# Performance work log

Hardware: AMD Instinct MI355X
Metric: run time of the kernel (lower is better)

## Reference

```python
import jax, jax.numpy as jnp
import numpy as np

B = 64      # graphs per batch
N = 1024    # nodes per graph (equal-size graphs -> static top-k)
D = 256     # in_dim
DEG = 16    # avg degree
K = 512     # k = ratio * N, ratio = 0.5
E = B * N * DEG
NT = B * N


def setup_inputs() -> dict:
    key = jax.random.key(0)
    ks = jax.random.split(key, 8)
    feature = jax.random.normal(ks[0], (NT, D), jnp.float32)
    gid = jnp.repeat(jnp.arange(B), N * DEG)          # graph id per edge
    src = gid * N + jax.random.randint(ks[1], (E,), 0, N)
    dst = gid * N + jax.random.randint(ks[2], (E,), 0, N)
    label = jax.random.randint(ks[3], (B,), 0, 2)
    W = jax.random.normal(ks[4], (D, 1), jnp.float32) / np.sqrt(D)   # GraphConv weight
    b = jnp.zeros((1,), jnp.float32)                                  # GraphConv bias
    lin1_w = jax.random.normal(ks[5], (2, 1), jnp.float32) / np.sqrt(2.0)
    lin1_b = jnp.zeros((1,), jnp.float32)
    return dict(feature=feature, src=src, dst=dst, label=label,
                W=W, b=b, lin1_w=lin1_w, lin1_b=lin1_b)


def reference(feature, src, dst, label, W, b, lin1_w, lin1_b):
    fdt = feature.dtype
    # ---- get_bias_score: distance-to-class-center score ----
    node_label = jnp.repeat(label, N).astype(fdt)                 # [NT]
    gemb = feature.reshape(B, N, D).mean(axis=1)                  # AvgPooling per graph [B, D]
    lab_f = label.astype(fdt)                                     # [B]
    n1 = jnp.maximum(lab_f.sum(), 1.0)
    n0 = jnp.maximum((1.0 - lab_f).sum(), 1.0)
    center0 = (gemb * (1.0 - lab_f)[:, None]).sum(0) / n0         # [D]
    center1 = (gemb * lab_f[:, None]).sum(0) / n1                 # [D]
    d0 = jnp.sqrt(((feature - center0) ** 2).sum(-1))             # [NT]
    d1 = jnp.sqrt(((feature - center1) ** 2).sum(-1))             # [NT]
    score_distance = (d0 - d1) * ((node_label - 0.5) * 2.0)       # [NT]
    # ---- GraphConv(in_dim, 1), norm='both' (DGL semantics) ----
    ones_e = jnp.ones((E,), fdt)
    deg_out = jax.ops.segment_sum(ones_e, src, NT)
    deg_in = jax.ops.segment_sum(ones_e, dst, NT)
    ns = jnp.maximum(deg_out, 1.0) ** -0.5                        # src-side norm
    nd = jnp.maximum(deg_in, 1.0) ** -0.5                         # dst-side norm
    h = (feature @ W) * ns[:, None]                               # project first (out<in) [NT,1]
    agg = jax.ops.segment_sum(h[src], dst, NT)                    # [NT,1]
    score_gcn = (agg * nd[:, None] + b)[:, 0]                     # [NT]
    # ---- combine two scores with lin1: Linear(2, 1) ----
    score = jnp.stack([score_gcn, score_distance], axis=-1) @ lin1_w + lin1_b  # [NT,1]
    sflat = score[:, 0]
    # ---- per-graph top-k (mytopk with equal-size graphs -> static k) ----
    _, idx = jax.lax.top_k(sflat.reshape(B, N), K)                # [B,K] local indices
    perm = (idx + (jnp.arange(B) * N)[:, None]).reshape(-1)       # [B*K] global indices
    mask = jnp.ones((NT,), bool).at[perm].set(False)
    perm_com = jnp.nonzero(mask, size=NT - B * K)[0]              # complement, static size
    # ---- gather + tanh-gated features ----
    feature_dis = feature[perm] * jnp.tanh(sflat[perm])[:, None]          # [B*K, D]
    feature_com = feature[perm_com] * jnp.tanh(sflat[perm_com])[:, None]  # [B*(N-K), D]
    score_soft = jax.nn.softmax(score, axis=0)                    # softmax over all nodes
    return feature_dis, feature_com, perm, perm_com, score_soft
```

## Files before the change

### kernel.cpp

```cpp
#include <hip/hip_runtime.h>
#include <math.h>

#define Bg   64
#define Nn   1024
#define Dd   256
#define EPG  16384
#define NT   (Bg * Nn)
#define Kk   512

#define OFF_DIS   0
#define OFF_COM   8388608
#define OFF_PERM  16777216
#define OFF_PCOM  16809984
#define OFF_SOFT  16842752

#define WS_H0     0
#define WS_SFLAT  (NT * 4)
#define WS_GPART  (NT * 4 * 2)
#define WS_REDM   (WS_GPART + 512 * 256 * 4)
#define WS_REDS   (WS_REDM + 256)
#define WS_PERMI  (WS_REDS + 256)
#define WS_PCOMI  (WS_PERMI + 32768 * 4)

__global__ __launch_bounds__(256) void k_col(
        const float* __restrict__ f, const float* __restrict__ W,
        float* __restrict__ gpart, float* __restrict__ h0) {
    __shared__ float scol[1024];
    int blk = blockIdx.x, t = threadIdx.x;
    int base = blk * 128;
    int lane = t & 63, wid = t >> 6;
    const float4* f4 = (const float4*)f;
    const float4* W4 = (const float4*)W;
    float4 w = W4[lane];
    float4 cs = make_float4(0.f, 0.f, 0.f, 0.f);
    for (int r = 0; r < 32; ++r) {
        int row = base + wid * 32 + r;
        float4 v = f4[(size_t)row * 64 + lane];
        cs.x += v.x; cs.y += v.y; cs.z += v.z; cs.w += v.w;
        float d = v.x * w.x + v.y * w.y + v.z * w.z + v.w * w.w;
        for (int o = 32; o > 0; o >>= 1) d += __shfl_xor(d, o);
        if (lane == 0) h0[row] = d;
    }
    ((float4*)scol)[wid * 64 + lane] = cs;
    __syncthreads();
    gpart[blk * Dd + t] = scol[t] + scol[Dd + t] + scol[2 * Dd + t] + scol[3 * Dd + t];
}

__global__ __launch_bounds__(1024) void k_graph(
        const float* __restrict__ f, const int* __restrict__ src,
        const int* __restrict__ dst, const int* __restrict__ label,
        const float* __restrict__ h0, const float* __restrict__ gpart,
        const float* __restrict__ b, const float* __restrict__ lw,
        const float* __restrict__ lb, float* __restrict__ sflat,
        int* __restrict__ permI, int* __restrict__ pcomI,
        float* __restrict__ out, float* __restrict__ redM, float* __restrict__ redS) {
    __shared__ uint4 ep4[4096];
    __shared__ int   sdo[1024];
    __shared__ int   sdi[1024];
    __shared__ float shn[1024];
    __shared__ float ssc[1024];
    __shared__ float sc0[1024];
    __shared__ float sc1[1024];
    __shared__ float c0f[256];
    __shared__ float c1f[256];
    __shared__ float sfl[1024];
    __shared__ unsigned long long sk[1024];
    __shared__ int   sflag[1024];
    __shared__ int   swave[8];
    __shared__ float sred[33];

    int g = blockIdx.x, t = threadIdx.x;
    int lane = t & 63, w16 = t >> 6;

    sdo[t] = 0; sdi[t] = 0;
    __syncthreads();

    {
        const int4* s4 = (const int4*)(src + g * EPG);
        const int4* d4 = (const int4*)(dst + g * EPG);
        #pragma unroll
        for (int i = t; i < EPG / 4; i += 1024) {
            int4 ss = s4[i];
            int4 dd = d4[i];
            int s0 = ss.x & (Nn - 1), s1 = ss.y & (Nn - 1), s2 = ss.z & (Nn - 1), s3 = ss.w & (Nn - 1);
            int e0 = dd.x & (Nn - 1), e1 = dd.y & (Nn - 1), e2 = dd.z & (Nn - 1), e3 = dd.w & (Nn - 1);
            uint4 pk;
            pk.x = (unsigned)(s0 | (e0 << 16));
            pk.y = (unsigned)(s1 | (e1 << 16));
            pk.z = (unsigned)(s2 | (e2 << 16));
            pk.w = (unsigned)(s3 | (e3 << 16));
            ep4[i] = pk;
            atomicAdd(&sdo[s0], 1); atomicAdd(&sdo[s1], 1);
            atomicAdd(&sdo[s2], 1); atomicAdd(&sdo[s3], 1);
            atomicAdd(&sdi[e0], 1); atomicAdd(&sdi[e1], 1);
            atomicAdd(&sdi[e2], 1); atomicAdd(&sdi[e3], 1);
        }
    }
    __syncthreads();

    {
        int dg = sdo[t]; if (dg < 1) dg = 1;
        shn[t] = h0[g * Nn + t] / sqrtf((float)dg);
        ssc[t] = 0.f;
    }
    __syncthreads();

    #pragma unroll
    for (int i = t; i < EPG / 4; i += 1024) {
        uint4 pk = ep4[i];
        atomicAdd(&ssc[pk.x >> 16], shn[pk.x & 0xFFFF]);
        atomicAdd(&ssc[pk.y >> 16], shn[pk.y & 0xFFFF]);
        atomicAdd(&ssc[pk.z >> 16], shn[pk.z & 0xFFFF]);
        atomicAdd(&ssc[pk.w >> 16], shn[pk.w & 0xFFFF]);
    }
    __syncthreads();

    {
        int dg = sdi[t]; if (dg < 1) dg = 1;
        ssc[t] = ssc[t] / sqrtf((float)dg) + b[0];
        int col = t & 255, chunk = t >> 8;
        float a0 = 0.f, a1 = 0.f;
        for (int gg = chunk * 16; gg < chunk * 16 + 16; ++gg) {
            float v = 0.f;
            #pragma unroll
            for (int p = 0; p < 8; ++p) v += gpart[(gg * 8 + p) * Dd + col];
            if (label[gg]) a1 += v; else a0 += v;
        }
        sc0[t] = a0; sc1[t] = a1;
    }
    __syncthreads();
    if (t < Dd) {
        int n1 = 0;
        for (int gg = 0; gg < Bg; ++gg) n1 += label[gg];
        float fn1 = fmaxf((float)n1, 1.f);
        float fn0 = fmaxf((float)(Bg - n1), 1.f);
        float s0 = sc0[t] + sc0[256 + t] + sc0[512 + t] + sc0[768 + t];
        float s1 = sc1[t] + sc1[256 + t] + sc1[512 + t] + sc1[768 + t];
        c0f[t] = s0 * (1.f / (float)Nn) / fn0;
        c1f[t] = s1 * (1.f / (float)Nn) / fn1;
    }
    __syncthreads();

    {
        int rg = lane >> 4, sub = lane & 15;
        float4 c0r[4], c1r[4];
        #pragma unroll
        for (int it = 0; it < 4; ++it) {
            c0r[it] = ((const float4*)c0f)[it * 16 + sub];
            c1r[it] = ((const float4*)c1f)[it * 16 + sub];
        }
        float lw0 = lw[0], lw1 = lw[1], lb0 = lb[0];
        float sgn = label[g] ? 1.f : -1.f;
        const float4* f4 = (const float4*)f;
        for (int grp = 0; grp < 16; ++grp) {
            int row = w16 * 64 + grp * 4 + rg;
            size_t bofs = (size_t)(g * Nn + row) * 64;
            float a0 = 0.f, a1 = 0.f;
            #pragma unroll
            for (int it = 0; it < 4; ++it) {
                float4 v = f4[bofs + it * 16 + sub];
                float dx;
                dx = v.x - c0r[it].x; a0 += dx * dx;
                dx = v.y - c0r[it].y; a0 += dx * dx;
                dx = v.z - c0r[it].z; a0 += dx * dx;
                dx = v.w - c0r[it].w; a0 += dx * dx;
                dx = v.x - c1r[it].x; a1 += dx * dx;
                dx = v.y - c1r[it].y; a1 += dx * dx;
                dx = v.z - c1r[it].z; a1 += dx * dx;
                dx = v.w - c1r[it].w; a1 += dx * dx;
            }
            #pragma unroll
            for (int o = 1; o < 16; o <<= 1) {
                a0 += __shfl_xor(a0, o);
                a1 += __shfl_xor(a1, o);
            }
            if (sub == 0) {
                float sdist = (sqrtf(a0) - sqrtf(a1)) * sgn;
                float val = ssc[row] * lw0 + sdist * lw1 + lb0;
                sfl[row] = val;
                sflat[g * Nn + row] = val;
            }
        }
    }
    __syncthreads();

    {
        unsigned u = __float_as_uint(sfl[t]);
        unsigned ox = u ^ ((u >> 31) ? 0xFFFFFFFFu : 0x80000000u);
        sk[t] = ((unsigned long long)ox << 32) | (unsigned)(1023 - t);
    }
    __syncthreads();
    for (int k = 2; k <= 1024; k <<= 1) {
        for (int j = k >> 1; j > 0; j >>= 1) {
            if (t < 512) {
                int l = ((t & ~(j - 1)) << 1) | (t & (j - 1));
                int r = l | j;
                unsigned long long A = sk[l], Bk = sk[r];
                bool up = ((l & k) == 0);
                if ((A < Bk) == up) { sk[l] = Bk; sk[r] = A; }
            }
            __syncthreads();
        }
    }
    sflag[t] = 1;
    __syncthreads();
    if (t < 512) {
        int loc = 1023 - (int)(sk[t] & 0xFFFFFFFFu);
        sflag[loc] = 0;
        int gi = g * Nn + loc;
        permI[g * Kk + t] = gi;
        out[OFF_PERM + g * Kk + t] = (float)gi;
    }
    __syncthreads();
    int f0 = 0, f1 = 0, f2 = 0, inc = 0;
    if (t < 512) {
        f0 = sflag[2 * t]; f1 = sflag[2 * t + 1];
        f2 = f0 + f1; inc = f2;
        for (int o = 1; o < 64; o <<= 1) {
            int y = __shfl_up(inc, o);
            if (lane >= o) inc += y;
        }
        if (lane == 63) swave[w16] = inc;
    }
    __syncthreads();
    if (t < 8) {
        int a = swave[t];
        for (int o = 1; o < 8; o <<= 1) {
            int y = __shfl_up(a, o);
            if (t >= o) a += y;
        }
        swave[t] = a;
    }
    __syncthreads();
    if (t < 512) {
        int basep = ((w16 > 0) ? swave[w16 - 1] : 0) + (inc - f2);
        if (f0) {
            int gi = g * Nn + 2 * t;
            pcomI[g * Kk + basep] = gi;
            out[OFF_PCOM + g * Kk + basep] = (float)gi;
        }
        if (f1) {
            int pos = basep + f0;
            int gi = g * Nn + 2 * t + 1;
            pcomI[g * Kk + pos] = gi;
            out[OFF_PCOM + g * Kk + pos] = (float)gi;
        }
    }
    float v = sfl[t];
    float m = v;
    for (int o = 32; o > 0; o >>= 1) m = fmaxf(m, __shfl_xor(m, o));
    if (lane == 0) sred[w16] = m;
    __syncthreads();
    if (t < 16) {
        float a = sred[t];
        for (int o = 8; o > 0; o >>= 1) a = fmaxf(a, __shfl_xor(a, o));
        if (t == 0) sred[32] = a;
    }
    __syncthreads();
    float M = sred[32];
    float s = expf(v - M);
    for (int o = 32; o > 0; o >>= 1) s += __shfl_xor(s, o);
    if (lane == 0) sred[16 + w16] = s;
    __syncthreads();
    if (t < 16) {
        float a = sred[16 + t];
        for (int o = 8; o > 0; o >>= 1) a += __shfl_xor(a, o);
        if (t == 0) { redM[g] = M; redS[g] = a; }
    }
}

__global__ void k_write(const float* __restrict__ f, const int* __restrict__ permI,
                        const int* __restrict__ pcomI, const float* __restrict__ sflat,
                        const float* __restrict__ redM, const float* __restrict__ redS,
                        float* __restrict__ out) {
    __shared__ float sMS[2];
    int t = threadIdx.x;
    if (t < 64) {
        float m = redM[t];
        float mm = m;
        for (int o = 32; o > 0; o >>= 1) mm = fmaxf(mm, __shfl_xor(mm, o));
        float s = redS[t] * expf(m - mm);
        for (int o = 32; o > 0; o >>= 1) s += __shfl_xor(s, o);
        if (t == 0) { sMS[0] = mm; sMS[1] = s; }
    }
    __syncthreads();
    float M = sMS[0], S = sMS[1];
    if (t < 4) {
        int i = blockIdx.x * 4 + t;
        out[OFF_SOFT + i] = expf(sflat[i] - M) / S;
    }
    int j = blockIdx.x * 4 + (t >> 6);
    int lane = t & 63;
    int row = (j < 32768) ? permI[j] : pcomI[j - 32768];
    float tv = tanhf(sflat[row]);
    const float4* f4 = (const float4*)f;
    float4* o4 = (float4*)out;
    float4 v = f4[(size_t)row * 64 + lane];
    o4[(size_t)j * 64 + lane] = make_float4(v.x * tv, v.y * tv, v.z * tv, v.w * tv);
}

extern "C" void kernel_launch(void* const* d_in, const int* in_sizes, int n_in,
                              void* d_out, int out_size, void* d_ws, size_t ws_size,
                              hipStream_t stream) {
    const float* feature = (const float*)d_in[0];
    const int*   src     = (const int*)d_in[1];
    const int*   dst     = (const int*)d_in[2];
    const int*   label   = (const int*)d_in[3];
    const float* W       = (const float*)d_in[4];
    const float* b       = (const float*)d_in[5];
    const float* lw      = (const float*)d_in[6];
    const float* lb      = (const float*)d_in[7];
    float* out = (float*)d_out;
    char*  ws  = (char*)d_ws;

    float* h0    = (float*)(ws + WS_H0);
    float* sflat = (float*)(ws + WS_SFLAT);
    float* gpart = (float*)(ws + WS_GPART);
    float* redM  = (float*)(ws + WS_REDM);
    float* redS  = (float*)(ws + WS_REDS);
    int*   permI = (int*)(ws + WS_PERMI);
    int*   pcomI = (int*)(ws + WS_PCOMI);

    k_col  <<<512,    256,  0, stream>>>(feature, W, gpart, h0);
    k_graph<<<Bg,     1024, 0, stream>>>(feature, src, dst, label, h0, gpart,
                                         b, lw, lb, sflat, permI, pcomI, out, redM, redS);
    k_write<<<NT / 4, 256,  0, stream>>>(feature, permI, pcomI, sflat, redM, redS, out);
}
```

Baseline: 214.7 us.

## Split monolithic per-graph kernel into edge, score, and top-k kernels

The 64-block per-graph kernel is split into three kernels. Edge aggregation stays per graph, while the class centers are computed once by block 0 instead of redundantly by every block. The distance-score pass, which streams the whole feature matrix, now runs as a grid of 4096 small blocks rather than 64 large ones, giving far more parallelism for the memory-bound read. Top-k and the softmax partials run in a 512-thread kernel with no idle threads. The cost is two extra launches and round-trips through workspace memory.

```diff
diff --git a/kernel.cpp b/kernel.cpp
--- a/kernel.cpp
+++ b/kernel.cpp
@@ -19,8 +19,11 @@
 #define WS_GPART  (NT * 4 * 2)
 #define WS_REDM   (WS_GPART + 512 * 256 * 4)
 #define WS_REDS   (WS_REDM + 256)
-#define WS_PERMI  (WS_REDS + 256)
+#define WS_C0     (WS_REDS + 256)
+#define WS_C1     (WS_C0 + 1024)
+#define WS_PERMI  (WS_C1 + 1024)
 #define WS_PCOMI  (WS_PERMI + 32768 * 4)
+#define WS_SGCN   (WS_PCOMI + 32768 * 4)
 
 __global__ __launch_bounds__(256) void k_col(
         const float* __restrict__ f, const float* __restrict__ W,
@@ -46,14 +49,11 @@
     gpart[blk * Dd + t] = scol[t] + scol[Dd + t] + scol[2 * Dd + t] + scol[3 * Dd + t];
 }
 
-__global__ __launch_bounds__(1024) void k_graph(
-        const float* __restrict__ f, const int* __restrict__ src,
-        const int* __restrict__ dst, const int* __restrict__ label,
-        const float* __restrict__ h0, const float* __restrict__ gpart,
-        const float* __restrict__ b, const float* __restrict__ lw,
-        const float* __restrict__ lb, float* __restrict__ sflat,
-        int* __restrict__ permI, int* __restrict__ pcomI,
-        float* __restrict__ out, float* __restrict__ redM, float* __restrict__ redS) {
+__global__ __launch_bounds__(1024) void k_edge(
+        const int* __restrict__ src, const int* __restrict__ dst,
+        const int* __restrict__ label, const float* __restrict__ h0,
+        const float* __restrict__ gpart, const float* __restrict__ b,
+        float* __restrict__ sgcn, float* __restrict__ c0, float* __restrict__ c1) {
     __shared__ uint4 ep4[4096];
     __shared__ int   sdo[1024];
     __shared__ int   sdi[1024];
@@ -61,18 +61,32 @@
     __shared__ float ssc[1024];
     __shared__ float sc0[1024];
     __shared__ float sc1[1024];
-    __shared__ float c0f[256];
-    __shared__ float c1f[256];
-    __shared__ float sfl[1024];
-    __shared__ unsigned long long sk[1024];
-    __shared__ int   sflag[1024];
-    __shared__ int   swave[8];
-    __shared__ float sred[33];
 
     int g = blockIdx.x, t = threadIdx.x;
-    int lane = t & 63, w16 = t >> 6;
-
     sdo[t] = 0; sdi[t] = 0;
+
+    if (g == 0) {
+        int col = t & 255, chunk = t >> 8;
+        float a0 = 0.f, a1 = 0.f;
+        for (int gg = chunk * 16; gg < chunk * 16 + 16; ++gg) {
+            float v = 0.f;
+            #pragma unroll
+            for (int p = 0; p < 8; ++p) v += gpart[(gg * 8 + p) * Dd + col];
+            if (label[gg]) a1 += v; else a0 += v;
+        }
+        sc0[t] = a0; sc1[t] = a1;
+        __syncthreads();
+        if (t < Dd) {
+            int n1 = 0;
+            for (int gg = 0; gg < Bg; ++gg) n1 += label[gg];
+            float fn1 = fmaxf((float)n1, 1.f);
+            float fn0 = fmaxf((float)(Bg - n1), 1.f);
+            float s0 = sc0[t] + sc0[256 + t] + sc0[512 + t] + sc0[768 + t];
+            float s1 = sc1[t] + sc1[256 + t] + sc1[512 + t] + sc1[768 + t];
+            c0[t] = s0 * (1.f / (float)Nn) / fn0;
+            c1[t] = s1 * (1.f / (float)Nn) / fn1;
+        }
+    }
     __syncthreads();
 
     {
@@ -117,94 +131,85 @@
 
     {
         int dg = sdi[t]; if (dg < 1) dg = 1;
-        ssc[t] = ssc[t] / sqrtf((float)dg) + b[0];
-        int col = t & 255, chunk = t >> 8;
-        float a0 = 0.f, a1 = 0.f;
-        for (int gg = chunk * 16; gg < chunk * 16 + 16; ++gg) {
-            float v = 0.f;
-            #pragma unroll
-            for (int p = 0; p < 8; ++p) v += gpart[(gg * 8 + p) * Dd + col];
-            if (label[gg]) a1 += v; else a0 += v;
-        }
-        sc0[t] = a0; sc1[t] = a1;
-    }
-    __syncthreads();
-    if (t < Dd) {
-        int n1 = 0;
-        for (int gg = 0; gg < Bg; ++gg) n1 += label[gg];
-        float fn1 = fmaxf((float)n1, 1.f);
-        float fn0 = fmaxf((float)(Bg - n1), 1.f);
-        float s0 = sc0[t] + sc0[256 + t] + sc0[512 + t] + sc0[768 + t];
-        float s1 = sc1[t] + sc1[256 + t] + sc1[512 + t] + sc1[768 + t];
-        c0f[t] = s0 * (1.f / (float)Nn) / fn0;
-        c1f[t] = s1 * (1.f / (float)Nn) / fn1;
-    }
-    __syncthreads();
-
-    {
-        int rg = lane >> 4, sub = lane & 15;
-        float4 c0r[4], c1r[4];
-        #pragma unroll
-        for (int it = 0; it < 4; ++it) {
-            c0r[it] = ((const float4*)c0f)[it * 16 + sub];
-            c1r[it] = ((const float4*)c1f)[it * 16 + sub];
-        }
-        float lw0 = lw[0], lw1 = lw[1], lb0 = lb[0];
+        sgcn[g * Nn + t] = ssc[t] / sqrtf((float)dg) + b[0];
+    }
+}
+
+__global__ __launch_bounds__(256) void k_score(
+        const float* __restrict__ f, const float* __restrict__ c0,
+        const float* __restrict__ c1, const float* __restrict__ sgcn,
+        const int* __restrict__ label, const float* __restrict__ lw,
+        const float* __restrict__ lb, float* __restrict__ sflat) {
+    int t = threadIdx.x;
+    int grp = t >> 4, sub = t & 15;
+    int row = blockIdx.x * 16 + grp;
+    int g = row >> 10;
+    const float4* f4 = (const float4*)f;
+    float4 c0r[4], c1r[4];
+    #pragma unroll
+    for (int it = 0; it < 4; ++it) {
+        c0r[it] = ((const float4*)c0)[it * 16 + sub];
+        c1r[it] = ((const float4*)c1)[it * 16 + sub];
+    }
+    float a0 = 0.f, a1 = 0.f;
+    size_t bofs = (size_t)row * 64;
+    #pragma unroll
+    for (int it = 0; it < 4; ++it) {
+        float4 v = f4[bofs + it * 16 + sub];
+        float dx;
+        dx = v.x - c0r[it].x; a0 += dx * dx;
+        dx = v.y - c0r[it].y; a0 += dx * dx;
+        dx = v.z - c0r[it].z; a0 += dx * dx;
+        dx = v.w - c0r[it].w; a0 += dx * dx;
+        dx = v.x - c1r[it].x; a1 += dx * dx;
+        dx = v.y - c1r[it].y; a1 += dx * dx;
+        dx = v.z - c1r[it].z; a1 += dx * dx;
+        dx = v.w - c1r[it].w; a1 += dx * dx;
+    }
+    #pragma unroll
+    for (int o = 1; o < 16; o <<= 1) {
+        a0 += __shfl_xor(a0, o);
+        a1 += __shfl_xor(a1, o);
+    }
+    if (sub == 0) {
         float sgn = label[g] ? 1.f : -1.f;
-        const float4* f4 = (const float4*)f;
-        for (int grp = 0; grp < 16; ++grp) {
-            int row = w16 * 64 + grp * 4 + rg;
-            size_t bofs = (size_t)(g * Nn + row) * 64;
-            float a0 = 0.f, a1 = 0.f;
-            #pragma unroll
-            for (int it = 0; it < 4; ++it) {
-                float4 v = f4[bofs + it * 16 + sub];
-                float dx;
-                dx = v.x - c0r[it].x; a0 += dx * dx;
-                dx = v.y - c0r[it].y; a0 += dx * dx;
-                dx = v.z - c0r[it].z; a0 += dx * dx;
-                dx = v.w - c0r[it].w; a0 += dx * dx;
-                dx = v.x - c1r[it].x; a1 += dx * dx;
-                dx = v.y - c1r[it].y; a1 += dx * dx;
-                dx = v.z - c1r[it].z; a1 += dx * dx;
-                dx = v.w - c1r[it].w; a1 += dx * dx;
-            }
-            #pragma unroll
-            for (int o = 1; o < 16; o <<= 1) {
-                a0 += __shfl_xor(a0, o);
-                a1 += __shfl_xor(a1, o);
-            }
-            if (sub == 0) {
-                float sdist = (sqrtf(a0) - sqrtf(a1)) * sgn;
-                float val = ssc[row] * lw0 + sdist * lw1 + lb0;
-                sfl[row] = val;
-                sflat[g * Nn + row] = val;
-            }
-        }
-    }
-    __syncthreads();
-
-    {
-        unsigned u = __float_as_uint(sfl[t]);
-        unsigned ox = u ^ ((u >> 31) ? 0xFFFFFFFFu : 0x80000000u);
-        sk[t] = ((unsigned long long)ox << 32) | (unsigned)(1023 - t);
-    }
+        float sdist = (sqrtf(a0) - sqrtf(a1)) * sgn;
+        sflat[row] = sgcn[row] * lw[0] + sdist * lw[1] + lb[0];
+    }
+}
+
+__global__ __launch_bounds__(512) void k_topk(
+        const float* __restrict__ sflat, int* __restrict__ permI,
+        int* __restrict__ pcomI, float* __restrict__ out,
+        float* __restrict__ redM, float* __restrict__ redS) {
+    __shared__ unsigned long long sk[1024];
+    __shared__ int   sflag[1024];
+    __shared__ int   swave[8];
+    __shared__ float sred[16];
+    int g = blockIdx.x, t = threadIdx.x;
+    int lane = t & 63, w = t >> 6;
+    float v0 = sflat[g * Nn + t];
+    float v1 = sflat[g * Nn + t + 512];
+    unsigned u0 = __float_as_uint(v0);
+    unsigned u1 = __float_as_uint(v1);
+    unsigned o0 = u0 ^ ((u0 >> 31) ? 0xFFFFFFFFu : 0x80000000u);
+    unsigned o1 = u1 ^ ((u1 >> 31) ? 0xFFFFFFFFu : 0x80000000u);
+    sk[t]       = ((unsigned long long)o0 << 32) | (unsigned)(1023 - t);
+    sk[t + 512] = ((unsigned long long)o1 << 32) | (unsigned)(1023 - (t + 512));
     __syncthreads();
     for (int k = 2; k <= 1024; k <<= 1) {
         for (int j = k >> 1; j > 0; j >>= 1) {
-            if (t < 512) {
-                int l = ((t & ~(j - 1)) << 1) | (t & (j - 1));
-                int r = l | j;
-                unsigned long long A = sk[l], Bk = sk[r];
-                bool up = ((l & k) == 0);
-                if ((A < Bk) == up) { sk[l] = Bk; sk[r] = A; }
-            }
+            int l = ((t & ~(j - 1)) << 1) | (t & (j - 1));
+            int r = l | j;
+            unsigned long long a = sk[l], bk = sk[r];
+            bool up = ((l & k) == 0);
+            if ((a < bk) == up) { sk[l] = bk; sk[r] = a; }
             __syncthreads();
         }
     }
-    sflag[t] = 1;
-    __syncthreads();
-    if (t < 512) {
+    sflag[t] = 1; sflag[t + 512] = 1;
+    __syncthreads();
+    {
         int loc = 1023 - (int)(sk[t] & 0xFFFFFFFFu);
         sflag[loc] = 0;
         int gi = g * Nn + loc;
@@ -212,16 +217,14 @@
         out[OFF_PERM + g * Kk + t] = (float)gi;
     }
     __syncthreads();
-    int f0 = 0, f1 = 0, f2 = 0, inc = 0;
-    if (t < 512) {
-        f0 = sflag[2 * t]; f1 = sflag[2 * t + 1];
-        f2 = f0 + f1; inc = f2;
-        for (int o = 1; o < 64; o <<= 1) {
-            int y = __shfl_up(inc, o);
-            if (lane >= o) inc += y;
-        }
-        if (lane == 63) swave[w16] = inc;
-    }
+    int f0 = sflag[2 * t], f1 = sflag[2 * t + 1];
+    int f2 = f0 + f1;
+    int inc = f2;
+    for (int o = 1; o < 64; o <<= 1) {
+        int y = __shfl_up(inc, o);
+        if (lane >= o) inc += y;
+    }
+    if (lane == 63) swave[w] = inc;
     __syncthreads();
     if (t < 8) {
         int a = swave[t];
@@ -232,40 +235,37 @@
         swave[t] = a;
     }
     __syncthreads();
-    if (t < 512) {
-        int basep = ((w16 > 0) ? swave[w16 - 1] : 0) + (inc - f2);
-        if (f0) {
-            int gi = g * Nn + 2 * t;
-            pcomI[g * Kk + basep] = gi;
-            out[OFF_PCOM + g * Kk + basep] = (float)gi;
-        }
-        if (f1) {
-            int pos = basep + f0;
-            int gi = g * Nn + 2 * t + 1;
-            pcomI[g * Kk + pos] = gi;
-            out[OFF_PCOM + g * Kk + pos] = (float)gi;
-        }
-    }
-    float v = sfl[t];
-    float m = v;
+    int basep = ((w > 0) ? swave[w - 1] : 0) + (inc - f2);
+    if (f0) {
+        int gi = g * Nn + 2 * t;
+        pcomI[g * Kk + basep] = gi;
+        out[OFF_PCOM + g * Kk + basep] = (float)gi;
+    }
+    if (f1) {
+        int pos = basep + f0;
+        int gi = g * Nn + 2 * t + 1;
+        pcomI[g * Kk + pos] = gi;
+        out[OFF_PCOM + g * Kk + pos] = (float)gi;
+    }
+    float m = fmaxf(v0, v1);
     for (int o = 32; o > 0; o >>= 1) m = fmaxf(m, __shfl_xor(m, o));
-    if (lane == 0) sred[w16] = m;
-    __syncthreads();
-    if (t < 16) {
+    if (lane == 0) sred[w] = m;
+    __syncthreads();
+    if (t < 8) {
         float a = sred[t];
-        for (int o = 8; o > 0; o >>= 1) a = fmaxf(a, __shfl_xor(a, o));
-        if (t == 0) sred[32] = a;
-    }
-    __syncthreads();
-    float M = sred[32];
-    float s = expf(v - M);
+        for (int o = 4; o > 0; o >>= 1) a = fmaxf(a, __shfl_xor(a, o));
+        if (t == 0) sred[0] = a;
+    }
+    __syncthreads();
+    m = sred[0];
+    float s = expf(v0 - m) + expf(v1 - m);
     for (int o = 32; o > 0; o >>= 1) s += __shfl_xor(s, o);
-    if (lane == 0) sred[16 + w16] = s;
-    __syncthreads();
-    if (t < 16) {
-        float a = sred[16 + t];
-        for (int o = 8; o > 0; o >>= 1) a += __shfl_xor(a, o);
-        if (t == 0) { redM[g] = M; redS[g] = a; }
+    if (lane == 0) sred[8 + w] = s;
+    __syncthreads();
+    if (t < 8) {
+        float a = sred[8 + t];
+        for (int o = 4; o > 0; o >>= 1) a += __shfl_xor(a, o);
+        if (t == 0) { redM[g] = m; redS[g] = a; }
     }
 }
 
@@ -318,11 +318,15 @@
     float* gpart = (float*)(ws + WS_GPART);
     float* redM  = (float*)(ws + WS_REDM);
     float* redS  = (float*)(ws + WS_REDS);
+    float* c0    = (float*)(ws + WS_C0);
+    float* c1    = (float*)(ws + WS_C1);
     int*   permI = (int*)(ws + WS_PERMI);
     int*   pcomI = (int*)(ws + WS_PCOMI);
-
-    k_col  <<<512,    256,  0, stream>>>(feature, W, gpart, h0);
-    k_graph<<<Bg,     1024, 0, stream>>>(feature, src, dst, label, h0, gpart,
-                                         b, lw, lb, sflat, permI, pcomI, out, redM, redS);
-    k_write<<<NT / 4, 256,  0, stream>>>(feature, permI, pcomI, sflat, redM, redS, out);
-}
+    float* sgcn  = (float*)(ws + WS_SGCN);
+
+    k_col  <<<512,     256,  0, stream>>>(feature, W, gpart, h0);
+    k_edge <<<Bg,      1024, 0, stream>>>(src, dst, label, h0, gpart, b, sgcn, c0, c1);
+    k_score<<<NT / 16, 256,  0, stream>>>(feature, c0, c1, sgcn, label, lw, lb, sflat);
+    k_topk <<<Bg,      512,  0, stream>>>(sflat, permI, pcomI, out, redM, redS);
+    k_write<<<NT / 4,  256,  0, stream>>>(feature, permI, pcomI, sflat, redM, redS, out);
+}
```

Result: no change. 211.5 us (-1.5%).
